# Kernel optimization log

Hardware: AMD Instinct MI355X
Metric: run time of the kernel (lower is better)

The kernel has to match this reference:

```python
import jax, jax.numpy as jnp
import numpy as np

BLUR = 0.01
SQRT2 = np.sqrt(2.0).astype(np.float32)


def setup_inputs() -> dict:
    key = jax.random.key(0)
    ks = jax.random.split(key, 6)
    B, N, M, DF = 4, 4096, 4096, 16
    src = jax.random.normal(ks[0], (B, N, 3), dtype=jnp.float32)
    tgt = jax.random.normal(ks[1], (B, M, 3), dtype=jnp.float32)
    # small feature scale so C_ij / (2*blur^2) stays in a numerically sane range
    src_fea = jax.random.normal(ks[2], (B, N, DF), dtype=jnp.float32) * 0.01
    tgt_fea = jax.random.normal(ks[3], (B, M, DF), dtype=jnp.float32) * 0.01
    # dual potentials from the (opaque) Sinkhorn solve; O(blur^2) so F/blur^2 ~ O(1)
    F_i = jax.random.normal(ks[4], (B, N), dtype=jnp.float32) * (BLUR ** 2)
    G_j = jax.random.normal(ks[5], (B, M), dtype=jnp.float32) * (BLUR ** 2)
    return {"src": src, "tgt": tgt, "src_fea": src_fea, "tgt_fea": tgt_fea,
            "F_i": F_i, "G_j": G_j}


def _solve_rigid(x, y, w):
    # x: BxNxD points, y: BxNxD mapped points, w: BxNx1 weights
    B, N, D = x.shape
    sum_w = jnp.sum(w, axis=1, keepdims=True)                 # Bx1x1
    mu_x = jnp.sum(x * w, axis=1, keepdims=True) / sum_w      # Bx1xD
    mu_y = jnp.sum(y * w, axis=1, keepdims=True) / sum_w
    wx_hat = (x - mu_x) * w
    wy_hat = (y - mu_y) * w
    a = jnp.einsum('bnd,bne->bde', wy_hat, wx_hat)            # BxDxD = wy^T @ wx
    u, s, vh = jnp.linalg.svd(a)                              # a = u @ diag(s) @ vh
    v = jnp.swapaxes(vh, -1, -2)                              # torch.svd's V
    det = jnp.linalg.det(u @ v)                               # (B,)
    c = jnp.ones((B, D), dtype=x.dtype).at[:, -1].set(det)
    r = (u * c[:, :, None]) @ vh                              # (u*c) @ v^T
    t = mu_y - jnp.swapaxes(r @ jnp.swapaxes(mu_x, 1, 2), 1, 2)
    return r, t.reshape(B, D)


def reference(src, tgt, src_fea, tgt_fea, F_i, G_j):
    # weights are all ones -> log(a_i)=log(b_j)=0, weight1 divide is a no-op
    inv = 1.0 / (SQRT2 * BLUR)
    xx = src_fea * inv                                        # BxNxDf
    yy = tgt_fea * inv                                        # BxMxDf
    f_i = F_i / (BLUR ** 2)                                   # BxN
    g_j = G_j / (BLUR ** 2)                                   # BxM
    # C_ij = ||xx_i - yy_j||^2 via expansion
    x2 = jnp.sum(xx * xx, axis=-1)                            # BxN
    y2 = jnp.sum(yy * yy, axis=-1)                            # BxM
    xy = jnp.einsum('bnd,bmd->bnm', xx, yy)                   # BxNxM
    log_P = (f_i - x2)[:, :, None] + (g_j - y2)[:, None, :] + 2.0 * xy
    lse = jax.nn.logsumexp(log_P, axis=2)                     # BxN
    P_norm = jnp.exp(log_P - lse[:, :, None])                 # softmax over M
    mapped_position = jnp.einsum('bnm,bmd->bnd', P_norm, tgt) # sumsoftmaxweight
    mapped_mass_ratio = jnp.exp(lse)[:, :, None]              # exp(logP).sum(2)/1
    rotation, trans = _solve_rigid(src, mapped_position, mapped_mass_ratio)
    return rotation, trans
```

## Files before the change

kernel.cpp:

```cpp
#include <hip/hip_runtime.h>
#include <hip/hip_bf16.h>
#include <math.h>

#define BB 4
#define NN 4096
#define MM 4096
#define JC 64
#define CHUNK (MM / JC)
#define RR 4

#define INVF  70.71067811865475f
#define IB2   10000.0f
#define INV2  5000.0f
#define LOG2E 1.4426950408889634f
#define SCY   (INVF * 2.0f * LOG2E)

#define YT_F   0
#define PART_F (BB * MM * 20)
#define BLK_F  (PART_F + BB * JC * NN * 4)

typedef __attribute__((ext_vector_type(2))) float f32x2;
static __device__ __forceinline__ f32x2 fma2(f32x2 a, f32x2 b, f32x2 c) {
  return __builtin_elementwise_fma(a, b, c);
}

__global__ __launch_bounds__(256) void prep_kernel(
    const float* __restrict__ tgt_fea, const float* __restrict__ G_j,
    const float* __restrict__ tgt, float* __restrict__ ws) {
  int idx = blockIdx.x * 256 + threadIdx.x;
  const float4* tf = (const float4*)(tgt_fea + (size_t)idx * 16);
  float4 a[4];
  float ss = 0.f;
  #pragma unroll
  for (int k = 0; k < 4; ++k) {
    a[k] = tf[k];
    ss += a[k].x*a[k].x + a[k].y*a[k].y + a[k].z*a[k].z + a[k].w*a[k].w;
  }
  float y2n = ss * INV2;
  float gyl = LOG2E * (G_j[idx] * IB2 - y2n);
  float4* rec = (float4*)(ws + YT_F + (size_t)idx * 20);
  #pragma unroll
  for (int k = 0; k < 4; ++k)
    rec[k] = make_float4(a[k].x * SCY, a[k].y * SCY, a[k].z * SCY, a[k].w * SCY);
  rec[4] = make_float4(tgt[(size_t)idx*3+0], tgt[(size_t)idx*3+1],
                       tgt[(size_t)idx*3+2], gyl);
}

__global__ __launch_bounds__(256, 4) void attn_kernel(
    const float* __restrict__ src_fea, const float* __restrict__ ws,
    float* __restrict__ partial) {
  int tid = threadIdx.x;
  int b = blockIdx.z, jc = blockIdx.y;
  int ib = blockIdx.x * (256 * RR) + tid;

  f32x2 q2[RR][8];
  #pragma unroll
  for (int r = 0; r < RR; ++r) {
    const float4* sf = (const float4*)(src_fea
                     + ((size_t)b * NN + ib + 256 * r) * 16);
    #pragma unroll
    for (int k = 0; k < 4; ++k) {
      float4 v = sf[k];
      q2[r][2*k]   = (f32x2){ v.x * INVF, v.y * INVF };
      q2[r][2*k+1] = (f32x2){ v.z * INVF, v.w * INVF };
    }
  }

  const float* yt = ws + YT_F + ((size_t)b * MM + jc * CHUNK) * 20;
  f32x2 t01[RR], t2s[RR];
  #pragma unroll
  for (int r = 0; r < RR; ++r) { t01[r] = (f32x2){0.f,0.f}; t2s[r] = (f32x2){0.f,0.f}; }

  #pragma unroll 4
  for (int jj = 0; jj < CHUNK; ++jj) {
    const float4* y4 = (const float4*)(yt + jj * 20);
    float4 ya = y4[0], yb = y4[1], yc = y4[2], yd = y4[3], tg = y4[4];
    f32x2 yv0 = (f32x2){ya.x, ya.y}, yv1 = (f32x2){ya.z, ya.w};
    f32x2 yv2 = (f32x2){yb.x, yb.y}, yv3 = (f32x2){yb.z, yb.w};
    f32x2 yv4 = (f32x2){yc.x, yc.y}, yv5 = (f32x2){yc.z, yc.w};
    f32x2 yv6 = (f32x2){yd.x, yd.y}, yv7 = (f32x2){yd.z, yd.w};
    f32x2 bias = (f32x2){tg.w, 0.f};
    f32x2 tgxy = (f32x2){tg.x, tg.y};
    f32x2 tgz1 = (f32x2){tg.z, 1.f};
    #pragma unroll
    for (int r = 0; r < RR; ++r) {
      f32x2 cA = fma2(q2[r][0], yv0, bias);
      cA = fma2(q2[r][2], yv2, cA);
      cA = fma2(q2[r][4], yv4, cA);
      cA = fma2(q2[r][6], yv6, cA);
      f32x2 cB = q2[r][1] * yv1;
      cB = fma2(q2[r][3], yv3, cB);
      cB = fma2(q2[r][5], yv5, cB);
      cB = fma2(q2[r][7], yv7, cB);
      f32x2 cs = cA + cB;
      float p = __builtin_amdgcn_exp2f(cs.x + cs.y);
      f32x2 pp2 = (f32x2){p, p};
      t01[r] = fma2(pp2, tgxy, t01[r]);
      t2s[r] = fma2(pp2, tgz1, t2s[r]);
    }
  }

  float4* pp = (float4*)partial + (size_t)(b * JC + jc) * NN;
  #pragma unroll
  for (int r = 0; r < RR; ++r)
    pp[ib + 256 * r] = make_float4(t01[r].x, t01[r].y, t2s[r].x, t2s[r].y);
}

__global__ __launch_bounds__(256) void combine_kernel(
    const float* __restrict__ partial, const float* __restrict__ src_fea,
    const float* __restrict__ src, const float* __restrict__ F_i,
    double* __restrict__ blockpart) {
  int b = blockIdx.x, xb = blockIdx.y, tid = threadIdx.x;
  int i = xb * 256 + tid;
  int g = b * NN + i;

  float S = 0.f, T0 = 0.f, T1 = 0.f, T2 = 0.f;
  #pragma unroll 8
  for (int c = 0; c < JC; ++c) {
    float4 v = ((const float4*)partial)[(size_t)(b * JC + c) * NN + i];
    T0 += v.x; T1 += v.y; T2 += v.z; S += v.w;
  }
  float invS = 1.f / S;
  float y0 = T0 * invS, y1 = T1 * invS, y2 = T2 * invS;

  const float4* sfp = (const float4*)src_fea + (size_t)g * 4;
  float ss = 0.f;
  #pragma unroll
  for (int k = 0; k < 4; ++k) {
    float4 a = sfp[k];
    ss += a.x*a.x + a.y*a.y + a.z*a.z + a.w*a.w;
  }
  float x2 = ss * INV2;
  float w = __builtin_amdgcn_exp2f((F_i[g] * IB2 - x2) * LOG2E
                                   + __builtin_amdgcn_logf(S));

  float px = src[(size_t)g * 3 + 0];
  float py = src[(size_t)g * 3 + 1];
  float pz = src[(size_t)g * 3 + 2];

  double acc[23];
  double wd = (double)w, w2 = wd * wd;
  acc[0]  = wd;
  acc[1]  = wd * px;  acc[2]  = wd * py;  acc[3]  = wd * pz;
  acc[4]  = wd * y0;  acc[5]  = wd * y1;  acc[6]  = wd * y2;
  acc[7]  = w2;
  acc[8]  = w2 * px;  acc[9]  = w2 * py;  acc[10] = w2 * pz;
  acc[11] = w2 * y0;  acc[12] = w2 * y1;  acc[13] = w2 * y2;
  acc[14] = w2 * y0 * px; acc[15] = w2 * y0 * py; acc[16] = w2 * y0 * pz;
  acc[17] = w2 * y1 * px; acc[18] = w2 * y1 * py; acc[19] = w2 * y1 * pz;
  acc[20] = w2 * y2 * px; acc[21] = w2 * y2 * py; acc[22] = w2 * y2 * pz;

  #pragma unroll
  for (int k = 0; k < 23; ++k) {
    #pragma unroll
    for (int off = 32; off > 0; off >>= 1)
      acc[k] += __shfl_down(acc[k], off, 64);
  }
  __shared__ double red[4][23];
  int wave = tid >> 6, lane = tid & 63;
  if (lane == 0) {
    #pragma unroll
    for (int k = 0; k < 23; ++k) red[wave][k] = acc[k];
  }
  __syncthreads();
  if (tid < 23) {
    double s = red[0][tid] + red[1][tid] + red[2][tid] + red[3][tid];
    blockpart[((size_t)b * 16 + xb) * 23 + tid] = s;
  }
}

__device__ __forceinline__ double det3(const double M[3][3]) {
  return M[0][0] * (M[1][1] * M[2][2] - M[1][2] * M[2][1])
       - M[0][1] * (M[1][0] * M[2][2] - M[1][2] * M[2][0])
       + M[0][2] * (M[1][0] * M[2][1] - M[1][1] * M[2][0]);
}

__global__ void finalize_kernel(const double* __restrict__ blockpart,
                                float* __restrict__ out) {
  __shared__ double sm[BB][23];
  int tid = threadIdx.x;
  int b = tid >> 6, lane = tid & 63;
  if (lane < 23) {
    double s = 0.0;
    for (int xb = 0; xb < 16; ++xb)
      s += blockpart[((size_t)b * 16 + xb) * 23 + lane];
    sm[b][lane] = s;
  }
  __syncthreads();
  if (lane != 0) return;

  double mo[23];
  #pragma unroll
  for (int k = 0; k < 23; ++k) mo[k] = sm[b][k];

  double sw = mo[0];
  double mux[3] = { mo[1] / sw, mo[2] / sw, mo[3] / sw };
  double muy[3] = { mo[4] / sw, mo[5] / sw, mo[6] / sw };
  double sw2 = mo[7];
  double A[3][3];
  for (int d = 0; d < 3; ++d)
    for (int e = 0; e < 3; ++e)
      A[d][e] = mo[14 + d * 3 + e] - muy[d] * mo[8 + e] - mux[e] * mo[11 + d]
              + sw2 * muy[d] * mux[e];

  double ATA[3][3];
  for (int p = 0; p < 3; ++p)
    for (int q = 0; q < 3; ++q)
      ATA[p][q] = A[0][p] * A[0][q] + A[1][p] * A[1][q] + A[2][p] * A[2][q];

  double V[3][3] = { {1,0,0}, {0,1,0}, {0,0,1} };
  for (int sweep = 0; sweep < 8; ++sweep) {
    for (int pair = 0; pair < 3; ++pair) {
      int p = (pair == 2) ? 1 : 0;
      int q = (pair == 0) ? 1 : 2;
      double apq = ATA[p][q];
      if (fabs(apq) < 1e-300) continue;
      double tau = (ATA[q][q] - ATA[p][p]) / (2.0 * apq);
      double tt = ((tau >= 0.0) ? 1.0 : -1.0) / (fabs(tau) + sqrt(1.0 + tau * tau));
      double c = 1.0 / sqrt(1.0 + tt * tt), sn = tt * c;
      for (int k = 0; k < 3; ++k) {
        double akp = ATA[k][p], akq = ATA[k][q];
        ATA[k][p] = c * akp - sn * akq;
        ATA[k][q] = sn * akp + c * akq;
      }
      for (int k = 0; k < 3; ++k) {
        double apk = ATA[p][k], aqk = ATA[q][k];
        ATA[p][k] = c * apk - sn * aqk;
        ATA[q][k] = sn * apk + c * aqk;
      }
      for (int k = 0; k < 3; ++k) {
        double vkp = V[k][p], vkq = V[k][q];
        V[k][p] = c * vkp - sn * vkq;
        V[k][q] = sn * vkp + c * vkq;
      }
    }
  }

  double U[3][3];
  for (int k = 0; k < 3; ++k) {
    double sv = sqrt(fmax(ATA[k][k], 0.0));
    double u0 = A[0][0] * V[0][k] + A[0][1] * V[1][k] + A[0][2] * V[2][k];
    double u1 = A[1][0] * V[0][k] + A[1][1] * V[1][k] + A[1][2] * V[2][k];
    double u2 = A[2][0] * V[0][k] + A[2][1] * V[1][k] + A[2][2] * V[2][k];
    double inv = (sv > 1e-300) ? 1.0 / sv : 0.0;
    U[0][k] = u0 * inv; U[1][k] = u1 * inv; U[2][k] = u2 * inv;
  }

  double dd = det3(U) * det3(V);
  double R[3][3];
  for (int d = 0; d < 3; ++d)
    for (int e = 0; e < 3; ++e)
      R[d][e] = U[d][0] * V[e][0] + U[d][1] * V[e][1] + U[d][2] * V[e][2];
  R[2][0] *= dd; R[2][1] *= dd; R[2][2] *= dd;

  double tr[3];
  for (int d = 0; d < 3; ++d)
    tr[d] = muy[d] - (R[d][0] * mux[0] + R[d][1] * mux[1] + R[d][2] * mux[2]);

  for (int d = 0; d < 3; ++d)
    for (int e = 0; e < 3; ++e)
      out[b * 9 + d * 3 + e] = (float)R[d][e];
  out[BB * 9 + b * 3 + 0] = (float)tr[0];
  out[BB * 9 + b * 3 + 1] = (float)tr[1];
  out[BB * 9 + b * 3 + 2] = (float)tr[2];
}

extern "C" void kernel_launch(void* const* d_in, const int* in_sizes, int n_in,
                              void* d_out, int out_size, void* d_ws, size_t ws_size,
                              hipStream_t stream) {
  const float* src     = (const float*)d_in[0];
  const float* tgt     = (const float*)d_in[1];
  const float* src_fea = (const float*)d_in[2];
  const float* tgt_fea = (const float*)d_in[3];
  const float* F_i     = (const float*)d_in[4];
  const float* G_j     = (const float*)d_in[5];
  float* ws  = (float*)d_ws;
  float* out = (float*)d_out;
  double* blockpart = (double*)(ws + BLK_F);

  prep_kernel<<<BB * MM / 256, 256, 0, stream>>>(tgt_fea, G_j, tgt, ws);
  dim3 grid(NN / (256 * RR), JC, BB);
  attn_kernel<<<grid, 256, 0, stream>>>(src_fea, ws, ws + PART_F);
  dim3 cgrid(BB, NN / 256);
  combine_kernel<<<cgrid, 256, 0, stream>>>(ws + PART_F, src_fea, src, F_i, blockpart);
  finalize_kernel<<<1, 256, 0, stream>>>(blockpart, out);
}
```

Measured before the change: 134.5 us.

## Compute attention logits with split-bf16 MFMA instead of scalar packed FMAs

The feature dot products in the attention kernel move from per-thread packed FP32 FMAs to 32x32x16 bf16 MFMA instructions. To keep near-FP32 accuracy, each operand is split into high and low bf16 parts and three MFMAs are summed. The prep kernel now writes target features in an MFMA-friendly swizzled bf16 layout plus a separate float4 array of target positions and biases, both staged into shared memory. The grid also grows because each block now covers 256 source rows. The exp2 and weighted accumulation stay scalar and now read target data from LDS. This adds a cross-lane shuffle reduction, and the split-bf16 scheme risks small precision loss in the exponent.

```diff
diff --git a/kernel.cpp b/kernel.cpp
--- a/kernel.cpp
+++ b/kernel.cpp
@@ -7,7 +7,6 @@
 #define MM 4096
 #define JC 64
 #define CHUNK (MM / JC)
-#define RR 4
 
 #define INVF  70.71067811865475f
 #define IB2   10000.0f
@@ -15,95 +14,163 @@
 #define LOG2E 1.4426950408889634f
 #define SCY   (INVF * 2.0f * LOG2E)
 
-#define YT_F   0
-#define PART_F (BB * MM * 20)
+#define YF_F   0
+#define TG4_F  262144
+#define PART_F 327680
 #define BLK_F  (PART_F + BB * JC * NN * 4)
 
-typedef __attribute__((ext_vector_type(2))) float f32x2;
-static __device__ __forceinline__ f32x2 fma2(f32x2 a, f32x2 b, f32x2 c) {
-  return __builtin_elementwise_fma(a, b, c);
+typedef __attribute__((ext_vector_type(2)))  float f32x2;
+typedef __attribute__((ext_vector_type(8)))  short short8v;
+typedef __attribute__((ext_vector_type(16))) float f32x16;
+
+static __device__ __forceinline__ unsigned short f2bf(float x) {
+  unsigned int u = __builtin_bit_cast(unsigned int, x);
+  u += 0x7fffu + ((u >> 16) & 1u);
+  return (unsigned short)(u >> 16);
+}
+static __device__ __forceinline__ float bf2f(unsigned short h) {
+  unsigned int u = ((unsigned int)h) << 16;
+  return __builtin_bit_cast(float, u);
+}
+static __device__ __forceinline__ void splitbf(float v, unsigned short& h, unsigned short& l) {
+  h = f2bf(v);
+  l = f2bf(v - bf2f(h));
+}
+static __device__ __forceinline__ f32x2 pkfma(f32x2 a, f32x2 b, f32x2 c) {
+  f32x2 d;
+  asm("v_pk_fma_f32 %0, %1, %2, %3" : "=v"(d) : "v"(a), "v"(b), "v"(c));
+  return d;
 }
 
 __global__ __launch_bounds__(256) void prep_kernel(
     const float* __restrict__ tgt_fea, const float* __restrict__ G_j,
     const float* __restrict__ tgt, float* __restrict__ ws) {
   int idx = blockIdx.x * 256 + threadIdx.x;
+  int b = idx >> 12, j = idx & (MM - 1);
   const float4* tf = (const float4*)(tgt_fea + (size_t)idx * 16);
-  float4 a[4];
+  float f[16];
   float ss = 0.f;
   #pragma unroll
   for (int k = 0; k < 4; ++k) {
-    a[k] = tf[k];
-    ss += a[k].x*a[k].x + a[k].y*a[k].y + a[k].z*a[k].z + a[k].w*a[k].w;
+    float4 v = tf[k];
+    f[4*k+0] = v.x; f[4*k+1] = v.y; f[4*k+2] = v.z; f[4*k+3] = v.w;
+    ss += v.x*v.x + v.y*v.y + v.z*v.z + v.w*v.w;
   }
   float y2n = ss * INV2;
+
+  unsigned short vh[16], vl[16];
+  #pragma unroll
+  for (int k = 0; k < 16; ++k) splitbf(f[k] * SCY, vh[k], vl[k]);
+
+  uint4* base = (uint4*)(ws + YF_F) + ((size_t)b * (MM/32) + (j >> 5)) * 128;
+  int ll = j & 31, lh = 32 + (j & 31);
+  base[0*64 + ll] = make_uint4(
+      (unsigned)vh[0] | ((unsigned)vh[1] << 16), (unsigned)vh[2] | ((unsigned)vh[3] << 16),
+      (unsigned)vh[8] | ((unsigned)vh[9] << 16), (unsigned)vh[10] | ((unsigned)vh[11] << 16));
+  base[1*64 + ll] = make_uint4(
+      (unsigned)vl[0] | ((unsigned)vl[1] << 16), (unsigned)vl[2] | ((unsigned)vl[3] << 16),
+      (unsigned)vl[8] | ((unsigned)vl[9] << 16), (unsigned)vl[10] | ((unsigned)vl[11] << 16));
+  base[0*64 + lh] = make_uint4(
+      (unsigned)vh[4] | ((unsigned)vh[5] << 16), (unsigned)vh[6] | ((unsigned)vh[7] << 16),
+      (unsigned)vh[12] | ((unsigned)vh[13] << 16), (unsigned)vh[14] | ((unsigned)vh[15] << 16));
+  base[1*64 + lh] = make_uint4(
+      (unsigned)vl[4] | ((unsigned)vl[5] << 16), (unsigned)vl[6] | ((unsigned)vl[7] << 16),
+      (unsigned)vl[12] | ((unsigned)vl[13] << 16), (unsigned)vl[14] | ((unsigned)vl[15] << 16));
+
   float gyl = LOG2E * (G_j[idx] * IB2 - y2n);
-  float4* rec = (float4*)(ws + YT_F + (size_t)idx * 20);
-  #pragma unroll
-  for (int k = 0; k < 4; ++k)
-    rec[k] = make_float4(a[k].x * SCY, a[k].y * SCY, a[k].z * SCY, a[k].w * SCY);
-  rec[4] = make_float4(tgt[(size_t)idx*3+0], tgt[(size_t)idx*3+1],
-                       tgt[(size_t)idx*3+2], gyl);
+  ((float4*)(ws + TG4_F))[idx] = make_float4(
+      tgt[(size_t)idx*3+0], tgt[(size_t)idx*3+1], tgt[(size_t)idx*3+2], gyl);
 }
 
 __global__ __launch_bounds__(256, 4) void attn_kernel(
     const float* __restrict__ src_fea, const float* __restrict__ ws,
     float* __restrict__ partial) {
+  __shared__ uint4  sY[256];
+  __shared__ float4 tg4s[CHUNK];
   int tid = threadIdx.x;
+  int w = tid >> 6, l = tid & 63;
+  int il = l & 31, h = l >> 5;
   int b = blockIdx.z, jc = blockIdx.y;
-  int ib = blockIdx.x * (256 * RR) + tid;
-
-  f32x2 q2[RR][8];
-  #pragma unroll
-  for (int r = 0; r < RR; ++r) {
-    const float4* sf = (const float4*)(src_fea
-                     + ((size_t)b * NN + ib + 256 * r) * 16);
+
+  {
+    const uint4* gY = (const uint4*)(ws + YF_F)
+                    + ((size_t)b * (MM/32) + jc * 2) * 128;
+    sY[tid] = gY[tid];
+    if (tid < CHUNK)
+      tg4s[tid] = ((const float4*)(ws + TG4_F))[(size_t)b * MM + jc * CHUNK + tid];
+  }
+
+  int i0 = blockIdx.x * 256 + w * 64;
+  union U { uint4 q; short8v s; };
+  U xaH, xaL, xbH, xbL;
+  #pragma unroll
+  for (int t = 0; t < 2; ++t) {
+    const float* sf = src_fea + ((size_t)b * NN + i0 + t * 32 + il) * 16;
+    float xv[16];
     #pragma unroll
     for (int k = 0; k < 4; ++k) {
-      float4 v = sf[k];
-      q2[r][2*k]   = (f32x2){ v.x * INVF, v.y * INVF };
-      q2[r][2*k+1] = (f32x2){ v.z * INVF, v.w * INVF };
+      float4 v = *(const float4*)(sf + 4 * k);
+      xv[4*k+0] = v.x * INVF; xv[4*k+1] = v.y * INVF;
+      xv[4*k+2] = v.z * INVF; xv[4*k+3] = v.w * INVF;
     }
-  }
-
-  const float* yt = ws + YT_F + ((size_t)b * MM + jc * CHUNK) * 20;
-  f32x2 t01[RR], t2s[RR];
-  #pragma unroll
-  for (int r = 0; r < RR; ++r) { t01[r] = (f32x2){0.f,0.f}; t2s[r] = (f32x2){0.f,0.f}; }
-
-  #pragma unroll 4
-  for (int jj = 0; jj < CHUNK; ++jj) {
-    const float4* y4 = (const float4*)(yt + jj * 20);
-    float4 ya = y4[0], yb = y4[1], yc = y4[2], yd = y4[3], tg = y4[4];
-    f32x2 yv0 = (f32x2){ya.x, ya.y}, yv1 = (f32x2){ya.z, ya.w};
-    f32x2 yv2 = (f32x2){yb.x, yb.y}, yv3 = (f32x2){yb.z, yb.w};
-    f32x2 yv4 = (f32x2){yc.x, yc.y}, yv5 = (f32x2){yc.z, yc.w};
-    f32x2 yv6 = (f32x2){yd.x, yd.y}, yv7 = (f32x2){yd.z, yd.w};
-    f32x2 bias = (f32x2){tg.w, 0.f};
-    f32x2 tgxy = (f32x2){tg.x, tg.y};
-    f32x2 tgz1 = (f32x2){tg.z, 1.f};
-    #pragma unroll
-    for (int r = 0; r < RR; ++r) {
-      f32x2 cA = fma2(q2[r][0], yv0, bias);
-      cA = fma2(q2[r][2], yv2, cA);
-      cA = fma2(q2[r][4], yv4, cA);
-      cA = fma2(q2[r][6], yv6, cA);
-      f32x2 cB = q2[r][1] * yv1;
-      cB = fma2(q2[r][3], yv3, cB);
-      cB = fma2(q2[r][5], yv5, cB);
-      cB = fma2(q2[r][7], yv7, cB);
-      f32x2 cs = cA + cB;
-      float p = __builtin_amdgcn_exp2f(cs.x + cs.y);
-      f32x2 pp2 = (f32x2){p, p};
-      t01[r] = fma2(pp2, tgxy, t01[r]);
-      t2s[r] = fma2(pp2, tgz1, t2s[r]);
+    unsigned short qh[8], ql[8];
+    #pragma unroll
+    for (int kk = 0; kk < 4; ++kk) {
+      splitbf(xv[4*h + kk],     qh[kk],   ql[kk]);
+      splitbf(xv[8 + 4*h + kk], qh[4+kk], ql[4+kk]);
     }
-  }
-
-  float4* pp = (float4*)partial + (size_t)(b * JC + jc) * NN;
-  #pragma unroll
-  for (int r = 0; r < RR; ++r)
-    pp[ib + 256 * r] = make_float4(t01[r].x, t01[r].y, t2s[r].x, t2s[r].y);
+    uint4 UH = make_uint4((unsigned)qh[0] | ((unsigned)qh[1] << 16),
+                          (unsigned)qh[2] | ((unsigned)qh[3] << 16),
+                          (unsigned)qh[4] | ((unsigned)qh[5] << 16),
+                          (unsigned)qh[6] | ((unsigned)qh[7] << 16));
+    uint4 UL = make_uint4((unsigned)ql[0] | ((unsigned)ql[1] << 16),
+                          (unsigned)ql[2] | ((unsigned)ql[3] << 16),
+                          (unsigned)ql[4] | ((unsigned)ql[5] << 16),
+                          (unsigned)ql[6] | ((unsigned)ql[7] << 16));
+    if (t == 0) { xaH.q = UH; xaL.q = UL; } else { xbH.q = UH; xbL.q = UL; }
+  }
+
+  __syncthreads();
+
+  f32x2 t01a = {0.f,0.f}, t2sa = {0.f,0.f};
+  f32x2 t01b = {0.f,0.f}, t2sb = {0.f,0.f};
+
+  #pragma unroll
+  for (int jt = 0; jt < 2; ++jt) {
+    U yH, yL;
+    yH.q = sY[jt * 128 + l];
+    yL.q = sY[jt * 128 + 64 + l];
+    f32x16 z = {};
+    f32x16 c1a = __builtin_amdgcn_mfma_f32_32x32x16_bf16(yL.s, xaH.s, z, 0, 0, 0);
+    c1a = __builtin_amdgcn_mfma_f32_32x32x16_bf16(yH.s, xaL.s, c1a, 0, 0, 0);
+    c1a = __builtin_amdgcn_mfma_f32_32x32x16_bf16(yH.s, xaH.s, c1a, 0, 0, 0);
+    f32x16 c1b = __builtin_amdgcn_mfma_f32_32x32x16_bf16(yL.s, xbH.s, z, 0, 0, 0);
+    c1b = __builtin_amdgcn_mfma_f32_32x32x16_bf16(yH.s, xbL.s, c1b, 0, 0, 0);
+    c1b = __builtin_amdgcn_mfma_f32_32x32x16_bf16(yH.s, xbH.s, c1b, 0, 0, 0);
+
+    #pragma unroll
+    for (int r = 0; r < 16; ++r) {
+      int jl = (r & 3) + 8 * (r >> 2) + (h << 2) + jt * 32;
+      float4 tg = tg4s[jl];
+      float pa = __builtin_amdgcn_exp2f(c1a[r] + tg.w);
+      float pb = __builtin_amdgcn_exp2f(c1b[r] + tg.w);
+      f32x2 pa2 = (f32x2){pa, pa}, pb2 = (f32x2){pb, pb};
+      f32x2 txy = (f32x2){tg.x, tg.y}, tz1 = (f32x2){tg.z, 1.f};
+      t01a = pkfma(pa2, txy, t01a); t2sa = pkfma(pa2, tz1, t2sa);
+      t01b = pkfma(pb2, txy, t01b); t2sb = pkfma(pb2, tz1, t2sb);
+    }
+  }
+
+  t01a.x += __shfl_xor(t01a.x, 32, 64); t01a.y += __shfl_xor(t01a.y, 32, 64);
+  t2sa.x += __shfl_xor(t2sa.x, 32, 64); t2sa.y += __shfl_xor(t2sa.y, 32, 64);
+  t01b.x += __shfl_xor(t01b.x, 32, 64); t01b.y += __shfl_xor(t01b.y, 32, 64);
+  t2sb.x += __shfl_xor(t2sb.x, 32, 64); t2sb.y += __shfl_xor(t2sb.y, 32, 64);
+
+  if (h == 0) {
+    float4* pp = (float4*)partial + (size_t)(b * JC + jc) * NN;
+    pp[i0 + il]      = make_float4(t01a.x, t01a.y, t2sa.x, t2sa.y);
+    pp[i0 + 32 + il] = make_float4(t01b.x, t01b.y, t2sb.x, t2sb.y);
+  }
 }
 
 __global__ __launch_bounds__(256) void combine_kernel(
@@ -279,7 +346,7 @@
   double* blockpart = (double*)(ws + BLK_F);
 
   prep_kernel<<<BB * MM / 256, 256, 0, stream>>>(tgt_fea, G_j, tgt, ws);
-  dim3 grid(NN / (256 * RR), JC, BB);
+  dim3 grid(NN / 256, JC, BB);
   attn_kernel<<<grid, 256, 0, stream>>>(src_fea, ws, ws + PART_F);
   dim3 cgrid(BB, NN / 256);
   combine_kernel<<<cgrid, 256, 0, stream>>>(ws + PART_F, src_fea, src, F_i, blockpart);
```

New measurement: 129.0 us. 1.04x faster.
